# Optimization experiments

Measured on AMD Instinct MI355X. Metric: run time of the kernel, lower is better.

## Reference

```python
import jax, jax.numpy as jnp
import numpy as np

S, B, C = 14, 2, 20          # grid size, boxes per cell, classes
LAMBDA_COORD, LAMBDA_NOOBJ = 5.0, 0.5
NCH = 5 * B + C              # 30 channels


def setup_inputs() -> dict:
    key = jax.random.key(0)
    k1, k2, k3 = jax.random.split(key, 3)
    Nb = 4096
    # positive values: loss takes sqrt(w), sqrt(h)
    pred = jax.random.uniform(k1, (Nb, S, S, NCH), dtype=jnp.float32, minval=0.05, maxval=1.0)
    target = jax.random.uniform(k2, (Nb, S, S, NCH), dtype=jnp.float32, minval=0.05, maxval=1.0)
    # binarize conf channels so coord (conf>0) / noobj (conf==0) partition the cells
    objf = (jax.random.uniform(k3, (Nb, S, S)) < 0.3).astype(jnp.float32)
    for b in range(B):
        target = target.at[..., 4 + 5 * b].set(objf)
    return {"pred_tensor": pred, "target_tensor": target}


def _to_xyxy(box):
    # box [..., 5] (or [..., B, 5]): cell-relative x,y and global w,h -> corners
    xy = box[..., :2] / S
    half = 0.5 * box[..., 2:4]
    return jnp.concatenate([xy - half, xy + half], axis=-1)


def reference(pred_tensor, target_tensor):
    pred, target = pred_tensor, target_tensor
    obj = (target[..., 4] > 0).astype(pred.dtype)      # [Nb,S,S]
    noobj = (target[..., 4] == 0).astype(pred.dtype)   # [Nb,S,S]

    pb = pred[..., :5 * B].reshape(pred.shape[:3] + (B, 5))     # [Nb,S,S,B,5]
    tb = target[..., :5 * B].reshape(target.shape[:3] + (B, 5))  # [Nb,S,S,B,5]

    # no-object confidence loss: conf channel of every box slot in noobj cells
    loss_noobj = jnp.sum(noobj[..., None] * (pb[..., 4] - tb[..., 4]) ** 2)

    # IoU of each of B predicted boxes vs the (first) target box of the cell
    pxy = _to_xyxy(pb)                        # [Nb,S,S,B,4]
    txy = _to_xyxy(tb[..., 0, :])[..., None, :]  # [Nb,S,S,1,4]
    lt = jnp.maximum(pxy[..., :2], txy[..., :2])
    rb = jnp.minimum(pxy[..., 2:], txy[..., 2:])
    wh = jnp.clip(rb - lt, 0.0)
    inter = wh[..., 0] * wh[..., 1]           # [Nb,S,S,B]
    area_p = (pxy[..., 2] - pxy[..., 0]) * (pxy[..., 3] - pxy[..., 1])
    area_t = (txy[..., 2] - txy[..., 0]) * (txy[..., 3] - txy[..., 1])
    iou = inter / (area_p + area_t - inter)

    max_iou = jax.lax.stop_gradient(jnp.max(iou, axis=-1))  # torch uses .data (detach)
    r = jnp.argmax(iou, axis=-1)              # responsible box index [Nb,S,S]

    pr = jnp.take_along_axis(pb, r[..., None, None], axis=3)[..., 0, :]  # [Nb,S,S,5]
    tr = jnp.take_along_axis(tb, r[..., None, None], axis=3)[..., 0, :]

    m = obj
    loss_xy = jnp.sum(m[..., None] * (pr[..., :2] - tr[..., :2]) ** 2)
    # guard sqrt in masked-out cells (values there don't matter)
    safe_pwh = jnp.where(m[..., None] > 0, pr[..., 2:4], 1.0)
    safe_twh = jnp.where(m[..., None] > 0, tr[..., 2:4], 1.0)
    loss_wh = jnp.sum(m[..., None] * (jnp.sqrt(safe_pwh) - jnp.sqrt(safe_twh)) ** 2)
    loss_obj = jnp.sum(m * (pr[..., 4] - max_iou) ** 2)
    loss_class = jnp.sum(m[..., None] * (pred[..., 5 * B:] - target[..., 5 * B:]) ** 2)

    loss = LAMBDA_COORD * (loss_xy + loss_wh) + loss_obj + LAMBDA_NOOBJ * loss_noobj + loss_class
    return loss / pred.shape[0]
```

## Files before the change

kernel.cpp:

```cpp
#include <hip/hip_runtime.h>


#define NB 4096
#define NCELL (NB * 14 * 14)
#define CELLS_PER_WAVE 64
#define NTILES (NCELL / CELLS_PER_WAVE)
#define WAVES_PER_BLOCK 4
#define NBLOCKS (NTILES / WAVES_PER_BLOCK)
#define TILE_FLOATS (CELLS_PER_WAVE * 30)
#define TILE_F4 (TILE_FLOATS / 4)

__device__ __forceinline__ void wave_fence() {
    __asm volatile("" ::: "memory");
    __builtin_amdgcn_wave_barrier();
    __asm volatile("" ::: "memory");
}

__global__ __launch_bounds__(256, 4) void yolo_partial(
    const float* __restrict__ pred, const float* __restrict__ target,
    float* __restrict__ partial)
{
    __shared__ float buf[WAVES_PER_BLOCK][TILE_FLOATS];

    const int lane = threadIdx.x & 63;
    const int wid  = threadIdx.x >> 6;
    const int tile = blockIdx.x * WAVES_PER_BLOCK + wid;
    float* wbuf = buf[wid];
    const size_t base4 = (size_t)tile * TILE_F4;

    const float4* pred4 = (const float4*)pred;
    const float4* targ4 = (const float4*)target;

    float4 pv[8], tv[8];
#pragma unroll
    for (int r = 0; r < 8; ++r) {
        int idx = r * 64 + lane;
        if (idx < TILE_F4) pv[r] = pred4[base4 + idx];
    }
#pragma unroll
    for (int r = 0; r < 8; ++r) {
        int idx = r * 64 + lane;
        if (idx < TILE_F4) tv[r] = targ4[base4 + idx];
    }

#pragma unroll
    for (int r = 0; r < 8; ++r) {
        int idx = r * 64 + lane;
        if (idx < TILE_F4) *(float4*)(wbuf + idx * 4) = pv[r];
    }
    wave_fence();

    float p[30];
    {
        const float2* s2 = (const float2*)(wbuf + lane * 30);
#pragma unroll
        for (int i = 0; i < 15; ++i) {
            float2 a = s2[i]; p[2 * i] = a.x; p[2 * i + 1] = a.y;
        }
    }
    wave_fence();

#pragma unroll
    for (int r = 0; r < 8; ++r) {
        int idx = r * 64 + lane;
        if (idx < TILE_F4) *(float4*)(wbuf + idx * 4) = tv[r];
    }
    wave_fence();

    float t[10];
    float cls = 0.0f;
    {
        const float2* s2 = (const float2*)(wbuf + lane * 30);
#pragma unroll
        for (int i = 0; i < 5; ++i) {
            float2 a = s2[i]; t[2 * i] = a.x; t[2 * i + 1] = a.y;
        }
#pragma unroll
        for (int i = 5; i < 15; ++i) {
            float2 a = s2[i];
            float d0 = p[2 * i] - a.x, d1 = p[2 * i + 1] - a.y;
            cls += d0 * d0 + d1 * d1;
        }
    }

    float loss;
    {
        const float t4 = t[4];
        const bool obj = (t4 > 0.0f);

        float dn0 = p[4] - t[4];
        float dn1 = p[9] - t[9];
        float noobj_l = (t4 == 0.0f) ? (dn0 * dn0 + dn1 * dn1) : 0.0f;

        const float invS = 1.0f / 14.0f;
        float tcx = t[0] * invS, tcy = t[1] * invS;
        float tx1 = tcx - 0.5f * t[2], ty1 = tcy - 0.5f * t[3];
        float tx2 = tcx + 0.5f * t[2], ty2 = tcy + 0.5f * t[3];
        float area_t = (tx2 - tx1) * (ty2 - ty1);

        float iou[2];
#pragma unroll
        for (int b = 0; b < 2; ++b) {
            const float* pb = p + 5 * b;
            float cx = pb[0] * invS, cy = pb[1] * invS;
            float x1 = cx - 0.5f * pb[2], y1 = cy - 0.5f * pb[3];
            float x2 = cx + 0.5f * pb[2], y2 = cy + 0.5f * pb[3];
            float lx = fmaxf(x1, tx1), ly = fmaxf(y1, ty1);
            float rx = fminf(x2, tx2), ry = fminf(y2, ty2);
            float wx = fmaxf(rx - lx, 0.0f), wy = fmaxf(ry - ly, 0.0f);
            float inter = wx * wy;
            float area_p = (x2 - x1) * (y2 - y1);
            iou[b] = inter / (area_p + area_t - inter);
        }

        int r = (iou[1] > iou[0]) ? 1 : 0;
        float max_iou = fmaxf(iou[0], iou[1]);

        float obj_l = 0.0f;
        if (obj) {
            const float* pr = p + 5 * r;
            const float* tr = t + 5 * r;
            float dx = pr[0] - tr[0], dy = pr[1] - tr[1];
            float lxy = dx * dx + dy * dy;
            float dw = sqrtf(pr[2]) - sqrtf(tr[2]);
            float dh = sqrtf(pr[3]) - sqrtf(tr[3]);
            float lwh = dw * dw + dh * dh;
            float dob = pr[4] - max_iou;
            float lob = dob * dob;
            obj_l = 5.0f * (lxy + lwh) + lob + cls;
        }
        loss = obj_l + 0.5f * noobj_l;
    }

    float v = loss;
#pragma unroll
    for (int off = 32; off > 0; off >>= 1)
        v += __shfl_down(v, off, 64);
    if (lane == 0)
        partial[tile] = v;
}

__global__ __launch_bounds__(256) void yolo_finalize(
    const float* __restrict__ partial, float* __restrict__ out)
{
    double s = 0.0;
    for (int i = threadIdx.x; i < NTILES; i += 256)
        s += (double)partial[i];

    __shared__ double sh[256];
    sh[threadIdx.x] = s;
    __syncthreads();
#pragma unroll
    for (int step = 128; step > 0; step >>= 1) {
        if (threadIdx.x < step) sh[threadIdx.x] += sh[threadIdx.x + step];
        __syncthreads();
    }
    if (threadIdx.x == 0)
        out[0] = (float)(sh[0] / (double)NB);
}

extern "C" void kernel_launch(void* const* d_in, const int* in_sizes, int n_in,
                              void* d_out, int out_size, void* d_ws, size_t ws_size,
                              hipStream_t stream) {
    const float* pred = (const float*)d_in[0];
    const float* target = (const float*)d_in[1];
    float* out = (float*)d_out;
    float* partial = (float*)d_ws;

    yolo_partial<<<NBLOCKS, 256, 0, stream>>>(pred, target, partial);
    yolo_finalize<<<1, 256, 0, stream>>>(partial, out);
}
```

Before: 220.6 us.

## Use persistent waves with register double-buffered prefetch of next tile

Replaces the one-tile-per-wave launch with 768 persistent blocks whose waves stride over tiles. The loads for the next tile go into registers while the current tile is staged through LDS and computed, so memory latency is hidden behind compute. Partial sums are accumulated per wave, which shrinks the finalize reduction. Occupancy hint drops to 3 blocks per CU to make room for the extra live registers, at the cost of fewer resident waves to hide latency.

```diff
diff --git a/kernel.cpp b/kernel.cpp
--- a/kernel.cpp
+++ b/kernel.cpp
@@ -3,11 +3,11 @@
 
 #define NB 4096
 #define NCELL (NB * 14 * 14)
-#define CELLS_PER_WAVE 64
-#define NTILES (NCELL / CELLS_PER_WAVE)
-#define WAVES_PER_BLOCK 4
-#define NBLOCKS (NTILES / WAVES_PER_BLOCK)
-#define TILE_FLOATS (CELLS_PER_WAVE * 30)
+#define NTILES (NCELL / 64)
+#define WPB 4
+#define NBLK 768
+#define NWAVES (NBLK * WPB)
+#define TILE_FLOATS (64 * 30)
 #define TILE_F4 (TILE_FLOATS / 4)
 
 __device__ __forceinline__ void wave_fence() {
@@ -16,135 +16,163 @@
     __asm volatile("" ::: "memory");
 }
 
-__global__ __launch_bounds__(256, 4) void yolo_partial(
+__global__ __launch_bounds__(256, 3) void yolo_partial(
     const float* __restrict__ pred, const float* __restrict__ target,
     float* __restrict__ partial)
 {
-    __shared__ float buf[WAVES_PER_BLOCK][TILE_FLOATS];
+    __shared__ float buf[WPB][TILE_FLOATS];
 
     const int lane = threadIdx.x & 63;
     const int wid  = threadIdx.x >> 6;
-    const int tile = blockIdx.x * WAVES_PER_BLOCK + wid;
+    const int w    = blockIdx.x * WPB + wid;
     float* wbuf = buf[wid];
-    const size_t base4 = (size_t)tile * TILE_F4;
 
     const float4* pred4 = (const float4*)pred;
     const float4* targ4 = (const float4*)target;
 
+    float acc = 0.0f;
     float4 pv[8], tv[8];
-#pragma unroll
-    for (int r = 0; r < 8; ++r) {
-        int idx = r * 64 + lane;
-        if (idx < TILE_F4) pv[r] = pred4[base4 + idx];
+
+    {
+        const size_t b4 = (size_t)w * TILE_F4;
+#pragma unroll
+        for (int r = 0; r < 8; ++r) {
+            int idx = r * 64 + lane;
+            if (idx < TILE_F4) pv[r] = pred4[b4 + idx];
+        }
+#pragma unroll
+        for (int r = 0; r < 8; ++r) {
+            int idx = r * 64 + lane;
+            if (idx < TILE_F4) tv[r] = targ4[b4 + idx];
+        }
     }
-#pragma unroll
-    for (int r = 0; r < 8; ++r) {
-        int idx = r * 64 + lane;
-        if (idx < TILE_F4) tv[r] = targ4[base4 + idx];
+
+    int tile = w;
+    while (tile < NTILES) {
+        const int next = tile + NWAVES;
+        const size_t nb4 = (size_t)next * TILE_F4;
+
+#pragma unroll
+        for (int r = 0; r < 8; ++r) {
+            int idx = r * 64 + lane;
+            if (idx < TILE_F4) *(float4*)(wbuf + idx * 4) = pv[r];
+        }
+        wave_fence();
+
+        float p[30];
+        {
+            const float2* s2 = (const float2*)(wbuf + lane * 30);
+#pragma unroll
+            for (int i = 0; i < 15; ++i) {
+                float2 a = s2[i]; p[2 * i] = a.x; p[2 * i + 1] = a.y;
+            }
+        }
+        wave_fence();
+
+        if (next < NTILES) {
+#pragma unroll
+            for (int r = 0; r < 8; ++r) {
+                int idx = r * 64 + lane;
+                if (idx < TILE_F4) pv[r] = pred4[nb4 + idx];
+            }
+        }
+
+#pragma unroll
+        for (int r = 0; r < 8; ++r) {
+            int idx = r * 64 + lane;
+            if (idx < TILE_F4) *(float4*)(wbuf + idx * 4) = tv[r];
+        }
+
+        if (next < NTILES) {
+#pragma unroll
+            for (int r = 0; r < 8; ++r) {
+                int idx = r * 64 + lane;
+                if (idx < TILE_F4) tv[r] = targ4[nb4 + idx];
+            }
+        }
+        wave_fence();
+
+        float t[10];
+        float cls = 0.0f;
+        {
+            const float2* s2 = (const float2*)(wbuf + lane * 30);
+#pragma unroll
+            for (int i = 0; i < 5; ++i) {
+                float2 a = s2[i]; t[2 * i] = a.x; t[2 * i + 1] = a.y;
+            }
+#pragma unroll
+            for (int i = 5; i < 15; ++i) {
+                float2 a = s2[i];
+                float d0 = p[2 * i] - a.x, d1 = p[2 * i + 1] - a.y;
+                cls += d0 * d0 + d1 * d1;
+            }
+        }
+        wave_fence();
+
+        {
+            const float t4 = t[4];
+            const bool obj = (t4 > 0.0f);
+
+            float dn0 = p[4] - t[4];
+            float dn1 = p[9] - t[9];
+            float noobj_l = (t4 == 0.0f) ? (dn0 * dn0 + dn1 * dn1) : 0.0f;
+
+            const float invS = 1.0f / 14.0f;
+            float tcx = t[0] * invS, tcy = t[1] * invS;
+            float tx1 = tcx - 0.5f * t[2], ty1 = tcy - 0.5f * t[3];
+            float tx2 = tcx + 0.5f * t[2], ty2 = tcy + 0.5f * t[3];
+            float area_t = (tx2 - tx1) * (ty2 - ty1);
+
+            float iou[2];
+#pragma unroll
+            for (int b = 0; b < 2; ++b) {
+                const float* pb = p + 5 * b;
+                float cx = pb[0] * invS, cy = pb[1] * invS;
+                float x1 = cx - 0.5f * pb[2], y1 = cy - 0.5f * pb[3];
+                float x2 = cx + 0.5f * pb[2], y2 = cy + 0.5f * pb[3];
+                float lx = fmaxf(x1, tx1), ly = fmaxf(y1, ty1);
+                float rx = fminf(x2, tx2), ry = fminf(y2, ty2);
+                float wx = fmaxf(rx - lx, 0.0f), wy = fmaxf(ry - ly, 0.0f);
+                float inter = wx * wy;
+                float area_p = (x2 - x1) * (y2 - y1);
+                iou[b] = inter / (area_p + area_t - inter);
+            }
+
+            int r = (iou[1] > iou[0]) ? 1 : 0;
+            float max_iou = fmaxf(iou[0], iou[1]);
+
+            float obj_l = 0.0f;
+            if (obj) {
+                const float* pr = p + 5 * r;
+                const float* tr = t + 5 * r;
+                float dx = pr[0] - tr[0], dy = pr[1] - tr[1];
+                float lxy = dx * dx + dy * dy;
+                float dw = sqrtf(pr[2]) - sqrtf(tr[2]);
+                float dh = sqrtf(pr[3]) - sqrtf(tr[3]);
+                float lwh = dw * dw + dh * dh;
+                float dob = pr[4] - max_iou;
+                float lob = dob * dob;
+                obj_l = 5.0f * (lxy + lwh) + lob + cls;
+            }
+            acc += obj_l + 0.5f * noobj_l;
+        }
+
+        tile = next;
     }
 
-#pragma unroll
-    for (int r = 0; r < 8; ++r) {
-        int idx = r * 64 + lane;
-        if (idx < TILE_F4) *(float4*)(wbuf + idx * 4) = pv[r];
-    }
-    wave_fence();
-
-    float p[30];
-    {
-        const float2* s2 = (const float2*)(wbuf + lane * 30);
-#pragma unroll
-        for (int i = 0; i < 15; ++i) {
-            float2 a = s2[i]; p[2 * i] = a.x; p[2 * i + 1] = a.y;
-        }
-    }
-    wave_fence();
-
-#pragma unroll
-    for (int r = 0; r < 8; ++r) {
-        int idx = r * 64 + lane;
-        if (idx < TILE_F4) *(float4*)(wbuf + idx * 4) = tv[r];
-    }
-    wave_fence();
-
-    float t[10];
-    float cls = 0.0f;
-    {
-        const float2* s2 = (const float2*)(wbuf + lane * 30);
-#pragma unroll
-        for (int i = 0; i < 5; ++i) {
-            float2 a = s2[i]; t[2 * i] = a.x; t[2 * i + 1] = a.y;
-        }
-#pragma unroll
-        for (int i = 5; i < 15; ++i) {
-            float2 a = s2[i];
-            float d0 = p[2 * i] - a.x, d1 = p[2 * i + 1] - a.y;
-            cls += d0 * d0 + d1 * d1;
-        }
-    }
-
-    float loss;
-    {
-        const float t4 = t[4];
-        const bool obj = (t4 > 0.0f);
-
-        float dn0 = p[4] - t[4];
-        float dn1 = p[9] - t[9];
-        float noobj_l = (t4 == 0.0f) ? (dn0 * dn0 + dn1 * dn1) : 0.0f;
-
-        const float invS = 1.0f / 14.0f;
-        float tcx = t[0] * invS, tcy = t[1] * invS;
-        float tx1 = tcx - 0.5f * t[2], ty1 = tcy - 0.5f * t[3];
-        float tx2 = tcx + 0.5f * t[2], ty2 = tcy + 0.5f * t[3];
-        float area_t = (tx2 - tx1) * (ty2 - ty1);
-
-        float iou[2];
-#pragma unroll
-        for (int b = 0; b < 2; ++b) {
-            const float* pb = p + 5 * b;
-            float cx = pb[0] * invS, cy = pb[1] * invS;
-            float x1 = cx - 0.5f * pb[2], y1 = cy - 0.5f * pb[3];
-            float x2 = cx + 0.5f * pb[2], y2 = cy + 0.5f * pb[3];
-            float lx = fmaxf(x1, tx1), ly = fmaxf(y1, ty1);
-            float rx = fminf(x2, tx2), ry = fminf(y2, ty2);
-            float wx = fmaxf(rx - lx, 0.0f), wy = fmaxf(ry - ly, 0.0f);
-            float inter = wx * wy;
-            float area_p = (x2 - x1) * (y2 - y1);
-            iou[b] = inter / (area_p + area_t - inter);
-        }
-
-        int r = (iou[1] > iou[0]) ? 1 : 0;
-        float max_iou = fmaxf(iou[0], iou[1]);
-
-        float obj_l = 0.0f;
-        if (obj) {
-            const float* pr = p + 5 * r;
-            const float* tr = t + 5 * r;
-            float dx = pr[0] - tr[0], dy = pr[1] - tr[1];
-            float lxy = dx * dx + dy * dy;
-            float dw = sqrtf(pr[2]) - sqrtf(tr[2]);
-            float dh = sqrtf(pr[3]) - sqrtf(tr[3]);
-            float lwh = dw * dw + dh * dh;
-            float dob = pr[4] - max_iou;
-            float lob = dob * dob;
-            obj_l = 5.0f * (lxy + lwh) + lob + cls;
-        }
-        loss = obj_l + 0.5f * noobj_l;
-    }
-
-    float v = loss;
+    float v = acc;
 #pragma unroll
     for (int off = 32; off > 0; off >>= 1)
         v += __shfl_down(v, off, 64);
     if (lane == 0)
-        partial[tile] = v;
+        partial[w] = v;
 }
 
 __global__ __launch_bounds__(256) void yolo_finalize(
     const float* __restrict__ partial, float* __restrict__ out)
 {
     double s = 0.0;
-    for (int i = threadIdx.x; i < NTILES; i += 256)
+    for (int i = threadIdx.x; i < NWAVES; i += 256)
         s += (double)partial[i];
 
     __shared__ double sh[256];
@@ -167,6 +195,6 @@
     float* out = (float*)d_out;
     float* partial = (float*)d_ws;
 
-    yolo_partial<<<NBLOCKS, 256, 0, stream>>>(pred, target, partial);
+    yolo_partial<<<NBLK, 256, 0, stream>>>(pred, target, partial);
     yolo_finalize<<<1, 256, 0, stream>>>(partial, out);
 }
```

Result: slower. 249.4 us (+13.1%).
